# Optimization experiments

Hardware: AMD Instinct MI355X
Metric: run time of the kernel (lower is better)

Reference implementation:

```python
import jax, jax.numpy as jnp
from jax import lax
import numpy as np

LOGZERO = -1e10  # matches the repo's `logzero` sentinel


def setup_inputs() -> dict:
    key = jax.random.key(0)
    k1, k2, k3, k4 = jax.random.split(key, 4)
    bs, xmax, vocab, ymax = 32, 1024, 1000, 128
    # CTC log-probabilities (ctc_generator output is log_softmax in the repo)
    ctc_out = jax.nn.log_softmax(
        jax.random.normal(k1, (bs, xmax, vocab), jnp.float32), axis=-1)
    src_size = jax.random.randint(k2, (bs,), xmax // 2, xmax + 1)
    src_mask = (jnp.arange(xmax)[None, :] < src_size[:, None])[:, None, :]  # [bs,1,xmax] bool
    ys = jax.random.randint(k3, (bs, ymax), 1, vocab)   # non-blank labels
    ylens = jax.random.randint(k4, (bs,), ymax // 2, ymax + 1)
    return {"ctc_out": ctc_out, "src_mask": src_mask, "src_size": src_size,
            "ys": ys, "ylens": ylens, "blank": 0}


def reference(ctc_out, src_mask, src_size, ys, ylens, blank):
    bs, xmax, vocab = ctc_out.shape
    ymax = ys.shape[1]
    L = 2 * ymax + 1  # blank-interleaved path length

    # mask invalid frames to logzero (masked_fill in torch)
    lp = jnp.where(src_mask.transpose(0, 2, 1), ctc_out, LOGZERO)  # [bs,xmax,vocab]

    # blank-interleaved path: [blank, y1, blank, y2, ..., blank]
    path = jnp.full((bs, L), blank, dtype=ys.dtype).at[:, 1::2].set(ys)
    path_lens = 2 * ylens + 1

    # log-probs gathered along the path: [xmax, bs, L] (time-major for scan)
    lp_path = jnp.take_along_axis(
        lp, jnp.broadcast_to(path[:, None, :], (bs, xmax, L)), axis=2)
    lp_path = lp_path.transpose(1, 0, 2)

    same_tr = path[:, :-2] == path[:, 2:]                 # [bs, L-2]
    idx = jnp.arange(L)
    outside = idx[None, :] >= path_lens[:, None]          # [bs, L]

    alpha0 = jnp.full((bs, L), LOGZERO, jnp.float32).at[:, 0].set(0.0)

    def step(alpha, lp_t):
        m0 = alpha
        m1 = jnp.concatenate([jnp.full((bs, 1), LOGZERO, alpha.dtype), alpha[:, :-1]], axis=1)
        m2 = jnp.concatenate([jnp.full((bs, 2), LOGZERO, alpha.dtype),
                              jnp.where(same_tr, LOGZERO, alpha[:, :-2])], axis=1)
        mat = jnp.stack([m0, m1, m2])                     # [3, bs, L]
        max_prob = jnp.max(mat, axis=0)
        arg = jnp.argmax(mat, axis=0)
        bp_t = idx[None, :] - arg                          # back-pointer (path position)
        max_prob = jnp.where(outside, LOGZERO, max_prob)
        alpha_new = max_prob + lp_t
        return alpha_new, (alpha_new, bp_t)

    _, (alpha_hist, bp) = lax.scan(step, alpha0, lp_path)  # [xmax,bs,L] each
    alpha_full = jnp.concatenate([alpha0[None], alpha_hist], axis=0)  # [xmax+1,bs,L]

    b_idx = jnp.arange(bs)
    alpha_at = alpha_full[src_size, b_idx]                 # [bs, L] alpha at t = src_size
    s1 = alpha_at[b_idx, path_lens - 1]
    s2 = alpha_at[b_idx, path_lens - 2]
    start = jnp.where(s1 > s2, path_lens - 1, path_lens - 2)
    score = jnp.maximum(s1, s2)                            # best alignment log-prob per utt

    # vectorized backtrace over all batches (reverse scan over time)
    def back_step(carry, t):
        tt = jnp.minimum(t + 1, xmax - 1)
        prev = bp[tt, b_idx, carry]                        # bp[b, t+1, state_{t+1}]
        val = jnp.where(t == src_size - 1, start,
                        jnp.where(t < src_size - 1, prev, 0))
        return val, val

    ts = jnp.arange(xmax - 1, -1, -1)
    _, states_rev = lax.scan(back_step, jnp.zeros((bs,), start.dtype), ts)
    states = states_rev[::-1].T                            # [bs, xmax] path positions

    aligned = jnp.take_along_axis(path, states, axis=1)    # [bs, xmax] tokens
    shift = jnp.concatenate([jnp.zeros((bs, 1), aligned.dtype), aligned[:, :-1]], axis=1)
    aligned = jnp.where(aligned == shift, 0, aligned)      # collapse repeats to 0
    shift2 = jnp.concatenate([jnp.zeros((bs, 1), aligned.dtype), aligned[:, :-1]], axis=1)

    csum = jnp.cumsum((shift2 != blank).astype(jnp.int32), axis=1)  # [bs, xmax]
    tm = csum[:, None, :] == jnp.arange(ymax + 1)[None, :, None]    # [bs, ymax+1, xmax]
    last = tm[:, -1, :] & src_mask[:, 0, :]
    last = last.at[b_idx, src_size - 1].set(True)
    tm = tm.at[:, -1, :].set(last)
    trigger_mask = tm & src_mask                           # & x_mask from FaNat.forward

    return score, trigger_mask, ylens + 1
```

## Files before the change

kernel.cpp:

```cpp
#include <hip/hip_runtime.h>
#include <stdint.h>

#define LOGZERO (-1e10f)

static constexpr int BS    = 32;
static constexpr int XMAX  = 1024;
static constexpr int VOCAB = 1000;
static constexpr int YMAX  = 128;
static constexpr int NROWS = YMAX + 1;
static constexpr int CH    = 8;
static constexpr int NPROD = 8;
static constexpr int NWAVES = 1 + NPROD;
static constexpr int NPAIR = XMAX / 2;

__global__ __launch_bounds__(64 * NWAVES) void k_viterbi(
    const float* __restrict__ ctc, const int* __restrict__ src_size,
    const int* __restrict__ ys, const int* __restrict__ ylens,
    const int* __restrict__ blankp, int* __restrict__ csum_ws,
    float* __restrict__ out)
{
    __shared__ float buf[2][CH][256];
    __shared__ unsigned char  bpb[XMAX * 64];
    __shared__ unsigned char  bp256[XMAX];
    __shared__ unsigned short bp2[NPAIR * 64];
    __shared__ unsigned char  bp2_256[NPAIR];
    __shared__ unsigned short st_lds[XMAX];
    __shared__ int ysl[YMAX];

    const int b    = blockIdx.x;
    const int tid  = threadIdx.x;
    const int wid  = tid >> 6;
    const int lane = tid & 63;
    const int ss   = src_size[b];
    const int yl   = ylens[b];
    const int bv   = blankp[0];
    const int plen = 2 * yl + 1;
    const float LZ = LOGZERO;

    for (int j = tid; j < YMAX; j += 64 * NWAVES) ysl[j] = ys[b * YMAX + j];
    for (int t = tid; t < XMAX; t += 64 * NWAVES) st_lds[t] = 0;
    __syncthreads();

    const int nchunk = (ss + CH - 1) / CH;
    const float* baseg = ctc + (size_t)b * XMAX * VOCAB;

    int start = 0;

    if (wid == 0) {
        const bool al1 = (lane > 0) && (ysl[2 * lane] != ysl[2 * lane - 1]);
        const bool al3 = (ysl[2 * lane + 1] != ysl[2 * lane]);
        const bool o0 = (4 * lane     >= plen);
        const bool o1 = (4 * lane + 1 >= plen);
        const bool o2 = (4 * lane + 2 >= plen);
        const bool o3 = (4 * lane + 3 >= plen);
        const bool o4 = (256 >= plen);
        const int rotidx = (lane + 63) & 63;

        float a0 = (lane == 0) ? 0.0f : LZ;
        float a1 = LZ, a2 = LZ, a3 = LZ, a4 = LZ;

        for (int c = 0; c < nchunk; ++c) {
            __syncthreads();
            const int cb = c & 1;
            float4 q[CH];
            #pragma unroll
            for (int r = 0; r < CH; ++r)
                q[r] = *reinterpret_cast<const float4*>(&buf[cb][r][lane * 4]);
            #pragma unroll
            for (int r = 0; r < CH; ++r) {
                const int t = c * CH + r;
                if (t < ss) {
                    float rot = __shfl(a3, rotidx);
                    float p3 = (lane == 0) ? LZ : rot;
                    float m0 = a0; int g0 = 0; if (p3 > m0) { m0 = p3; g0 = 1; }
                    float m1 = a1; int g1 = 0; if (a0 > m1) { m1 = a0; g1 = 1; }
                    float sk1 = al1 ? p3 : LZ;  if (sk1 > m1) { m1 = sk1; g1 = 2; }
                    float m2 = a2; int g2 = 0; if (a1 > m2) { m2 = a1; g2 = 1; }
                    float m3 = a3; int g3 = 0; if (a2 > m3) { m3 = a2; g3 = 1; }
                    float sk3 = al3 ? a1 : LZ;  if (sk3 > m3) { m3 = sk3; g3 = 2; }
                    float m4 = a4; int g4 = 0; if (rot > m4) { m4 = rot; g4 = 1; }
                    a0 = (o0 ? LZ : m0) + q[r].x;
                    a1 = (o1 ? LZ : m1) + q[r].y;
                    a2 = (o2 ? LZ : m2) + q[r].z;
                    a3 = (o3 ? LZ : m3) + q[r].w;
                    a4 = (o4 ? LZ : m4) + q[r].x;
                    bpb[t * 64 + lane] =
                        (unsigned char)(g0 | (g1 << 2) | (g2 << 4) | (g3 << 6));
                    if (lane == 0) bp256[t] = (unsigned char)g4;
                }
            }
        }

        auto getA = [&](int idx) -> float {
            if (idx == 256) return __shfl(a4, 0);
            int k = idx & 3;
            float pick = (k == 0) ? a0 : (k == 1) ? a1 : (k == 2) ? a2 : a3;
            return __shfl(pick, idx >> 2);
        };
        const float s1v = getA(plen - 1), s2v = getA(plen - 2);
        const float score = (s1v > s2v) ? s1v : s2v;
        start = (s1v > s2v) ? (plen - 1) : (plen - 2);
        if (lane == 0) {
            out[b] = score;
            out[32 + (size_t)BS * NROWS * XMAX + b] = (float)(yl + 1);
        }
    } else {
        const int pr = wid - 1;
        const int tokA = ysl[2 * lane];
        const int tokB = ysl[2 * lane + 1];
        int t0 = pr; if (t0 >= ss) t0 = ss - 1;
        const float* r0 = baseg + (size_t)t0 * VOCAB;
        float vb = r0[bv], va = r0[tokA], vc = r0[tokB];
        for (int c = 0; c < nchunk; ++c) {
            *reinterpret_cast<float4*>(&buf[c & 1][pr][lane * 4]) =
                make_float4(vb, va, vb, vc);
            int tn = (c + 1) * CH + pr; if (tn >= ss) tn = ss - 1;
            const float* r = baseg + (size_t)tn * VOCAB;
            vb = r[bv]; va = r[tokA]; vc = r[tokB];
            __syncthreads();
        }
    }
    __syncthreads();

    const int pmax = (ss - 1) >> 1;
    for (int p = 1 + wid; p <= pmax; p += NWAVES) {
        int oOdd  = bpb[(2 * p + 1) * 64 + lane];
        int oEven = bpb[(2 * p) * 64 + lane];
        int uEven = (lane > 0) ? bpb[(2 * p) * 64 + lane - 1] : 0;
        int evenWin = uEven | (oEven << 8);
        unsigned int acc = 0;
        #pragma unroll
        for (int k = 0; k < 4; ++k) {
            int a1v = (oOdd >> (2 * k)) & 3;
            int sh  = 2 * k - 2 * a1v + 8;
            int a2v = (evenWin >> sh) & 3;
            acc |= (unsigned)(a1v | (a2v << 2)) << (4 * k);
        }
        bp2[p * 64 + lane] = (unsigned short)acc;
        int a16 = bp256[2 * p + 1];
        int a26 = (a16 == 0) ? bp256[2 * p] : ((bpb[(2 * p) * 64 + 63] >> 6) & 3);
        if (lane == 0) bp2_256[p] = (unsigned char)(a16 | (a26 << 2));
    }
    __syncthreads();

    if (tid == 0) {
        int s = start, tc = ss - 1;
        st_lds[tc] = (unsigned short)s;
        if ((tc & 1) == 0 && tc >= 1) {
            int arg;
            if (s == 256) arg = bp256[tc];
            else arg = (bpb[tc * 64 + (s >> 2)] >> ((s & 3) * 2)) & 3;
            s -= arg; --tc; st_lds[tc] = (unsigned short)s;
        }
        while (tc > 1) {
            int n;
            if (s == 256) n = bp2_256[tc >> 1];
            else n = (bp2[(tc >> 1) * 64 + (s >> 2)] >> ((s & 3) * 4)) & 0xF;
            int sA = s - (n & 3);
            int sB = sA - (n >> 2);
            st_lds[tc - 1] = (unsigned short)sA;
            st_lds[tc - 2] = (unsigned short)sB;
            s = sB; tc -= 2;
        }
        if (tc == 1) {
            int arg;
            if (s == 256) arg = bp256[1];
            else arg = (bpb[64 + (s >> 2)] >> ((s & 3) * 2)) & 3;
            s -= arg; st_lds[0] = (unsigned short)s;
        }
    }
    __syncthreads();

    if (wid == 0) {
        auto tok_lds = [&](int stv) -> int { return (stv & 1) ? ysl[stv >> 1] : bv; };
        const int t0c = lane * 16;
        int prev_raw = (t0c == 0) ? 0 : tok_lds(st_lds[t0c - 1]);
        int cnt = 0;
        int csl[16];
        #pragma unroll
        for (int i = 0; i < 16; ++i) {
            int raw = tok_lds(st_lds[t0c + i]);
            int ac = (raw == prev_raw) ? 0 : raw;
            prev_raw = raw;
            csl[i] = cnt;
            cnt += (ac != bv) ? 1 : 0;
        }
        int v = cnt;
        #pragma unroll
        for (int off = 1; off < 64; off <<= 1) {
            int u = __shfl_up(v, off);
            if (lane >= off) v += u;
        }
        const int base_c = v - cnt;
        int* co = csum_ws + b * XMAX + t0c;
        #pragma unroll
        for (int i = 0; i < 16; ++i) co[i] = base_c + csl[i];
    }
}

__global__ __launch_bounds__(256) void k_mask(
    const int* __restrict__ csum_ws, const int* __restrict__ src_size,
    float* __restrict__ out)
{
    int bj = blockIdx.x;
    int b = bj / NROWS, j = bj - b * NROWS;
    int ss = src_size[b];
    const int* cs = csum_ws + b * XMAX;
    float* orow = out + 32 + (size_t)bj * XMAX;
    int t = threadIdx.x * 4;
    float4 v;
    float* vp = &v.x;
    #pragma unroll
    for (int i = 0; i < 4; ++i) {
        int tt = t + i;
        int c = cs[tt];
        bool in = tt < ss;
        bool val;
        if (j < YMAX) val = (c == j) && in;
        else          val = ((c == YMAX) || (tt == ss - 1)) && in;
        vp[i] = val ? 1.0f : 0.0f;
    }
    *(float4*)(orow + t) = v;
}

extern "C" void kernel_launch(void* const* d_in, const int* in_sizes, int n_in,
                              void* d_out, int out_size, void* d_ws, size_t ws_size,
                              hipStream_t stream) {
    const float* ctc      = (const float*)d_in[0];
    const int*   src_size = (const int*)d_in[2];
    const int*   ys       = (const int*)d_in[3];
    const int*   ylens    = (const int*)d_in[4];
    const int*   blankp   = (const int*)d_in[5];
    float* out = (float*)d_out;
    int*   csum_ws = (int*)d_ws;

    k_viterbi<<<BS, 64 * NWAVES, 0, stream>>>(ctc, src_size, ys, ylens, blankp,
                                              csum_ws, out);
    k_mask<<<BS * NROWS, 256, 0, stream>>>(csum_ws, src_size, out);
}
```

Before: 354.4 us.

## Load emissions directly in the Viterbi wave with triple-buffered register prefetch

Removes the eight producer waves and the LDS double buffer. The single Viterbi wave now issues its own global gathers into three rotating register buffers, prefetching two chunks ahead, so the per-chunk __syncthreads barriers disappear. The a3 update is reordered so the cross-lane shuffle for the next step is issued early, and the backpointer for state 256 is packed as bits into g4pack. The cost is that load latency must now be hidden by the one wave's prefetch depth, and register pressure rises.

```diff
diff --git a/kernel.cpp b/kernel.cpp
--- a/kernel.cpp
+++ b/kernel.cpp
@@ -9,8 +9,7 @@
 static constexpr int YMAX  = 128;
 static constexpr int NROWS = YMAX + 1;
 static constexpr int CH    = 8;
-static constexpr int NPROD = 8;
-static constexpr int NWAVES = 1 + NPROD;
+static constexpr int NWAVES = 9;
 static constexpr int NPAIR = XMAX / 2;
 
 __global__ __launch_bounds__(64 * NWAVES) void k_viterbi(
@@ -19,9 +18,8 @@
     const int* __restrict__ blankp, int* __restrict__ csum_ws,
     float* __restrict__ out)
 {
-    __shared__ float buf[2][CH][256];
     __shared__ unsigned char  bpb[XMAX * 64];
-    __shared__ unsigned char  bp256[XMAX];
+    __shared__ unsigned char  g4pack[XMAX / CH];
     __shared__ unsigned short bp2[NPAIR * 64];
     __shared__ unsigned char  bp2_256[NPAIR];
     __shared__ unsigned short st_lds[XMAX];
@@ -41,14 +39,14 @@
     for (int t = tid; t < XMAX; t += 64 * NWAVES) st_lds[t] = 0;
     __syncthreads();
 
-    const int nchunk = (ss + CH - 1) / CH;
     const float* baseg = ctc + (size_t)b * XMAX * VOCAB;
-
     int start = 0;
 
     if (wid == 0) {
-        const bool al1 = (lane > 0) && (ysl[2 * lane] != ysl[2 * lane - 1]);
-        const bool al3 = (ysl[2 * lane + 1] != ysl[2 * lane]);
+        const int tokA = ysl[2 * lane];
+        const int tokB = ysl[2 * lane + 1];
+        const bool al1 = (lane > 0) && (tokA != ysl[2 * lane - 1]);
+        const bool al3 = (tokB != tokA);
         const bool o0 = (4 * lane     >= plen);
         const bool o1 = (4 * lane + 1 >= plen);
         const bool o2 = (4 * lane + 2 >= plen);
@@ -58,38 +56,73 @@
 
         float a0 = (lane == 0) ? 0.0f : LZ;
         float a1 = LZ, a2 = LZ, a3 = LZ, a4 = LZ;
-
-        for (int c = 0; c < nchunk; ++c) {
-            __syncthreads();
-            const int cb = c & 1;
-            float4 q[CH];
-            #pragma unroll
-            for (int r = 0; r < CH; ++r)
-                q[r] = *reinterpret_cast<const float4*>(&buf[cb][r][lane * 4]);
-            #pragma unroll
-            for (int r = 0; r < CH; ++r) {
-                const int t = c * CH + r;
-                if (t < ss) {
-                    float rot = __shfl(a3, rotidx);
-                    float p3 = (lane == 0) ? LZ : rot;
-                    float m0 = a0; int g0 = 0; if (p3 > m0) { m0 = p3; g0 = 1; }
-                    float m1 = a1; int g1 = 0; if (a0 > m1) { m1 = a0; g1 = 1; }
-                    float sk1 = al1 ? p3 : LZ;  if (sk1 > m1) { m1 = sk1; g1 = 2; }
-                    float m2 = a2; int g2 = 0; if (a1 > m2) { m2 = a1; g2 = 1; }
-                    float m3 = a3; int g3 = 0; if (a2 > m3) { m3 = a2; g3 = 1; }
-                    float sk3 = al3 ? a1 : LZ;  if (sk3 > m3) { m3 = sk3; g3 = 2; }
-                    float m4 = a4; int g4 = 0; if (rot > m4) { m4 = rot; g4 = 1; }
-                    a0 = (o0 ? LZ : m0) + q[r].x;
-                    a1 = (o1 ? LZ : m1) + q[r].y;
-                    a2 = (o2 ? LZ : m2) + q[r].z;
-                    a3 = (o3 ? LZ : m3) + q[r].w;
-                    a4 = (o4 ? LZ : m4) + q[r].x;
-                    bpb[t * 64 + lane] =
-                        (unsigned char)(g0 | (g1 << 2) | (g2 << 4) | (g3 << 6));
-                    if (lane == 0) bp256[t] = (unsigned char)g4;
-                }
-            }
-        }
+        float rotp = __shfl(a3, rotidx);
+
+        float bB0[CH], bA0[CH], bC0[CH];
+        float bB1[CH], bA1[CH], bC1[CH];
+        float bB2[CH], bA2[CH], bC2[CH];
+
+        const int nch = (ss + CH - 1) / CH;
+
+#define ISSUE(BB, BA, BC, cc) do {                                          \
+            _Pragma("unroll")                                               \
+            for (int r_ = 0; r_ < CH; ++r_) {                               \
+                int t_ = (cc) * CH + r_; if (t_ > ss - 1) t_ = ss - 1;      \
+                const float* rp_ = baseg + (size_t)t_ * VOCAB;              \
+                BB[r_] = rp_[bv]; BA[r_] = rp_[tokA]; BC[r_] = rp_[tokB];   \
+            } } while (0)
+
+#define PROC(BB, BA, BC, cc) do {                                           \
+            unsigned int g4acc_ = 0;                                        \
+            _Pragma("unroll")                                               \
+            for (int r_ = 0; r_ < CH; ++r_) {                               \
+                const int t_ = (cc) * CH + r_;                              \
+                if (t_ < ss) {                                              \
+                     \
+                    float m3 = a3; int g3 = 0;                              \
+                    if (a2 > m3) { m3 = a2; g3 = 1; }                       \
+                    float sk3 = al3 ? a1 : LZ;                              \
+                    if (sk3 > m3) { m3 = sk3; g3 = 2; }                     \
+                    float a3n = (o3 ? LZ : m3) + BC[r_];                    \
+                    float rot = rotp;                                       \
+                    rotp = __shfl(a3n, rotidx);          \
+                    float p3 = (lane == 0) ? LZ : rot;                      \
+                    float m0 = a0; int g0 = 0;                              \
+                    if (p3 > m0) { m0 = p3; g0 = 1; }                       \
+                    float m1 = a1; int g1 = 0;                              \
+                    if (a0 > m1) { m1 = a0; g1 = 1; }                       \
+                    float sk1 = al1 ? p3 : LZ;                              \
+                    if (sk1 > m1) { m1 = sk1; g1 = 2; }                     \
+                    float m2 = a2; int g2 = 0;                              \
+                    if (a1 > m2) { m2 = a1; g2 = 1; }                       \
+                    float m4 = a4; int g4 = 0;                              \
+                    if (rot > m4) { m4 = rot; g4 = 1; }                     \
+                    a0 = (o0 ? LZ : m0) + BB[r_];                           \
+                    a1 = (o1 ? LZ : m1) + BA[r_];                           \
+                    a2 = (o2 ? LZ : m2) + BB[r_];                           \
+                    a3 = a3n;                                               \
+                    a4 = (o4 ? LZ : m4) + BB[r_];                           \
+                    g4acc_ |= (unsigned)g4 << r_;                           \
+                    bpb[t_ * 64 + lane] =                                   \
+                        (unsigned char)(g0 | (g1 << 2) | (g2 << 4) | (g3 << 6)); \
+                }                                                           \
+            }                                                               \
+            if (lane == 0 && (cc) * CH < ss)                                \
+                g4pack[cc] = (unsigned char)g4acc_;                         \
+        } while (0)
+
+        ISSUE(bB0, bA0, bC0, 0);
+        ISSUE(bB1, bA1, bC1, 1);
+        for (int c = 0; c < nch; c += 3) {
+            ISSUE(bB2, bA2, bC2, c + 2);
+            PROC (bB0, bA0, bC0, c);
+            ISSUE(bB0, bA0, bC0, c + 3);
+            PROC (bB1, bA1, bC1, c + 1);
+            ISSUE(bB1, bA1, bC1, c + 4);
+            PROC (bB2, bA2, bC2, c + 2);
+        }
+#undef ISSUE
+#undef PROC
 
         auto getA = [&](int idx) -> float {
             if (idx == 256) return __shfl(a4, 0);
@@ -104,21 +137,6 @@
             out[b] = score;
             out[32 + (size_t)BS * NROWS * XMAX + b] = (float)(yl + 1);
         }
-    } else {
-        const int pr = wid - 1;
-        const int tokA = ysl[2 * lane];
-        const int tokB = ysl[2 * lane + 1];
-        int t0 = pr; if (t0 >= ss) t0 = ss - 1;
-        const float* r0 = baseg + (size_t)t0 * VOCAB;
-        float vb = r0[bv], va = r0[tokA], vc = r0[tokB];
-        for (int c = 0; c < nchunk; ++c) {
-            *reinterpret_cast<float4*>(&buf[c & 1][pr][lane * 4]) =
-                make_float4(vb, va, vb, vc);
-            int tn = (c + 1) * CH + pr; if (tn >= ss) tn = ss - 1;
-            const float* r = baseg + (size_t)tn * VOCAB;
-            vb = r[bv]; va = r[tokA]; vc = r[tokB];
-            __syncthreads();
-        }
     }
     __syncthreads();
 
@@ -137,8 +155,10 @@
             acc |= (unsigned)(a1v | (a2v << 2)) << (4 * k);
         }
         bp2[p * 64 + lane] = (unsigned short)acc;
-        int a16 = bp256[2 * p + 1];
-        int a26 = (a16 == 0) ? bp256[2 * p] : ((bpb[(2 * p) * 64 + 63] >> 6) & 3);
+        const int tOdd = 2 * p + 1, tEven = 2 * p;
+        int a16 = (g4pack[tOdd >> 3] >> (tOdd & 7)) & 1;
+        int a26 = (a16 == 0) ? ((g4pack[tEven >> 3] >> (tEven & 7)) & 1)
+                             : ((bpb[tEven * 64 + 63] >> 6) & 3);
         if (lane == 0) bp2_256[p] = (unsigned char)(a16 | (a26 << 2));
     }
     __syncthreads();
@@ -148,7 +168,7 @@
         st_lds[tc] = (unsigned short)s;
         if ((tc & 1) == 0 && tc >= 1) {
             int arg;
-            if (s == 256) arg = bp256[tc];
+            if (s == 256) arg = (g4pack[tc >> 3] >> (tc & 7)) & 1;
             else arg = (bpb[tc * 64 + (s >> 2)] >> ((s & 3) * 2)) & 3;
             s -= arg; --tc; st_lds[tc] = (unsigned short)s;
         }
@@ -164,7 +184,7 @@
         }
         if (tc == 1) {
             int arg;
-            if (s == 256) arg = bp256[1];
+            if (s == 256) arg = (g4pack[0] >> 1) & 1;
             else arg = (bpb[64 + (s >> 2)] >> ((s & 3) * 2)) & 3;
             s -= arg; st_lds[0] = (unsigned short)s;
         }
```

Measured after the change: 401.8 us. 13.4% more time.

## Shorten Viterbi critical path with early shuffle, bit-packed bp, deeper prefetch

Applied to the files above, without the earlier changes.

The recursion wave now computes the a3 update first and issues the cross-lane shuffle for the next timestep early, so the shuffle latency overlaps the remaining max/argmax work. The per-timestep lane-0 byte store for the extra state is replaced by one bit-packed byte per chunk. __syncthreads is replaced by raw s_barrier with explicit waitcnt handling. Producer waves double-buffer their global loads two chunks ahead to hide memory latency. Together these target the serial dependency chain and the barrier cost per chunk. The manual barrier and waitcnt handling is fragile and risks ordering bugs.

```diff
diff --git a/kernel.cpp b/kernel.cpp
--- a/kernel.cpp
+++ b/kernel.cpp
@@ -21,7 +21,7 @@
 {
     __shared__ float buf[2][CH][256];
     __shared__ unsigned char  bpb[XMAX * 64];
-    __shared__ unsigned char  bp256[XMAX];
+    __shared__ unsigned char  g4pack[XMAX / CH];
     __shared__ unsigned short bp2[NPAIR * 64];
     __shared__ unsigned char  bp2_256[NPAIR];
     __shared__ unsigned short st_lds[XMAX];
@@ -47,8 +47,10 @@
     int start = 0;
 
     if (wid == 0) {
-        const bool al1 = (lane > 0) && (ysl[2 * lane] != ysl[2 * lane - 1]);
-        const bool al3 = (ysl[2 * lane + 1] != ysl[2 * lane]);
+        const int tokA = ysl[2 * lane];
+        const int tokB = ysl[2 * lane + 1];
+        const bool al1 = (lane > 0) && (tokA != ysl[2 * lane - 1]);
+        const bool al3 = (tokB != tokA);
         const bool o0 = (4 * lane     >= plen);
         const bool o1 = (4 * lane + 1 >= plen);
         const bool o2 = (4 * lane + 2 >= plen);
@@ -58,37 +60,46 @@
 
         float a0 = (lane == 0) ? 0.0f : LZ;
         float a1 = LZ, a2 = LZ, a3 = LZ, a4 = LZ;
+        float rotp = __shfl(a3, rotidx);
 
         for (int c = 0; c < nchunk; ++c) {
-            __syncthreads();
+            __builtin_amdgcn_s_barrier();
+            asm volatile("" ::: "memory");
+            __builtin_amdgcn_sched_barrier(0);
             const int cb = c & 1;
             float4 q[CH];
             #pragma unroll
             for (int r = 0; r < CH; ++r)
                 q[r] = *reinterpret_cast<const float4*>(&buf[cb][r][lane * 4]);
+            unsigned int g4acc = 0;
             #pragma unroll
             for (int r = 0; r < CH; ++r) {
                 const int t = c * CH + r;
                 if (t < ss) {
-                    float rot = __shfl(a3, rotidx);
+                    float m3 = a3; int g3 = 0;
+                    if (a2 > m3) { m3 = a2; g3 = 1; }
+                    float sk3 = al3 ? a1 : LZ;
+                    if (sk3 > m3) { m3 = sk3; g3 = 2; }
+                    float a3n = (o3 ? LZ : m3) + q[r].w;
+                    float rot = rotp;
+                    rotp = __shfl(a3n, rotidx);
                     float p3 = (lane == 0) ? LZ : rot;
                     float m0 = a0; int g0 = 0; if (p3 > m0) { m0 = p3; g0 = 1; }
                     float m1 = a1; int g1 = 0; if (a0 > m1) { m1 = a0; g1 = 1; }
                     float sk1 = al1 ? p3 : LZ;  if (sk1 > m1) { m1 = sk1; g1 = 2; }
                     float m2 = a2; int g2 = 0; if (a1 > m2) { m2 = a1; g2 = 1; }
-                    float m3 = a3; int g3 = 0; if (a2 > m3) { m3 = a2; g3 = 1; }
-                    float sk3 = al3 ? a1 : LZ;  if (sk3 > m3) { m3 = sk3; g3 = 2; }
                     float m4 = a4; int g4 = 0; if (rot > m4) { m4 = rot; g4 = 1; }
                     a0 = (o0 ? LZ : m0) + q[r].x;
                     a1 = (o1 ? LZ : m1) + q[r].y;
                     a2 = (o2 ? LZ : m2) + q[r].z;
-                    a3 = (o3 ? LZ : m3) + q[r].w;
+                    a3 = a3n;
                     a4 = (o4 ? LZ : m4) + q[r].x;
+                    g4acc |= (unsigned)g4 << r;
                     bpb[t * 64 + lane] =
                         (unsigned char)(g0 | (g1 << 2) | (g2 << 4) | (g3 << 6));
-                    if (lane == 0) bp256[t] = (unsigned char)g4;
                 }
             }
+            if (lane == 0) g4pack[c] = (unsigned char)g4acc;
         }
 
         auto getA = [&](int idx) -> float {
@@ -110,14 +121,26 @@
         const int tokB = ysl[2 * lane + 1];
         int t0 = pr; if (t0 >= ss) t0 = ss - 1;
         const float* r0 = baseg + (size_t)t0 * VOCAB;
-        float vb = r0[bv], va = r0[tokA], vc = r0[tokB];
+        float vb0 = r0[bv], va0 = r0[tokA], vc0 = r0[tokB];
+        int t1 = CH + pr; if (t1 >= ss) t1 = ss - 1;
+        const float* r1 = baseg + (size_t)t1 * VOCAB;
+        float vb1 = r1[bv], va1 = r1[tokA], vc1 = r1[tokB];
         for (int c = 0; c < nchunk; ++c) {
-            *reinterpret_cast<float4*>(&buf[c & 1][pr][lane * 4]) =
-                make_float4(vb, va, vb, vc);
-            int tn = (c + 1) * CH + pr; if (tn >= ss) tn = ss - 1;
-            const float* r = baseg + (size_t)tn * VOCAB;
-            vb = r[bv]; va = r[tokA]; vc = r[tokB];
-            __syncthreads();
+            if (c & 1) {
+                *reinterpret_cast<float4*>(&buf[1][pr][lane * 4]) =
+                    make_float4(vb1, va1, vb1, vc1);
+                int tn = (c + 2) * CH + pr; if (tn >= ss) tn = ss - 1;
+                const float* r = baseg + (size_t)tn * VOCAB;
+                vb1 = r[bv]; va1 = r[tokA]; vc1 = r[tokB];
+            } else {
+                *reinterpret_cast<float4*>(&buf[0][pr][lane * 4]) =
+                    make_float4(vb0, va0, vb0, vc0);
+                int tn = (c + 2) * CH + pr; if (tn >= ss) tn = ss - 1;
+                const float* r = baseg + (size_t)tn * VOCAB;
+                vb0 = r[bv]; va0 = r[tokA]; vc0 = r[tokB];
+            }
+            asm volatile("s_waitcnt lgkmcnt(0)" ::: "memory");
+            __builtin_amdgcn_s_barrier();
         }
     }
     __syncthreads();
@@ -137,8 +160,10 @@
             acc |= (unsigned)(a1v | (a2v << 2)) << (4 * k);
         }
         bp2[p * 64 + lane] = (unsigned short)acc;
-        int a16 = bp256[2 * p + 1];
-        int a26 = (a16 == 0) ? bp256[2 * p] : ((bpb[(2 * p) * 64 + 63] >> 6) & 3);
+        const int tOdd = 2 * p + 1, tEven = 2 * p;
+        int a16 = (g4pack[tOdd >> 3] >> (tOdd & 7)) & 1;
+        int a26 = (a16 == 0) ? ((g4pack[tEven >> 3] >> (tEven & 7)) & 1)
+                             : ((bpb[tEven * 64 + 63] >> 6) & 3);
         if (lane == 0) bp2_256[p] = (unsigned char)(a16 | (a26 << 2));
     }
     __syncthreads();
@@ -148,7 +173,7 @@
         st_lds[tc] = (unsigned short)s;
         if ((tc & 1) == 0 && tc >= 1) {
             int arg;
-            if (s == 256) arg = bp256[tc];
+            if (s == 256) arg = (g4pack[tc >> 3] >> (tc & 7)) & 1;
             else arg = (bpb[tc * 64 + (s >> 2)] >> ((s & 3) * 2)) & 3;
             s -= arg; --tc; st_lds[tc] = (unsigned short)s;
         }
@@ -164,7 +189,7 @@
         }
         if (tc == 1) {
             int arg;
-            if (s == 256) arg = bp256[1];
+            if (s == 256) arg = (g4pack[0] >> 1) & 1;
             else arg = (bpb[64 + (s >> 2)] >> ((s & 3) * 2)) & 3;
             s -= arg; st_lds[0] = (unsigned short)s;
         }
```

Result: slower. 363.0 us (+2.4%).
